# Kernel optimization log

Measured on AMD Instinct MI355X. Metric: run time of the kernel, lower is better.

Reference implementation:

```python
import jax, jax.numpy as jnp
import numpy as np

N_NODES = 100000
N_EDGES = 1600000
VOCAB = 10000
HIDDEN = 128
EMB1 = 128
EMB2 = 128
L1 = 64
N_GRAPHS = 256


def setup_inputs() -> dict:
    key = jax.random.key(0)
    ks = jax.random.split(key, 16)
    inp = {
        "x": jax.random.randint(ks[0], (N_NODES,), 0, VOCAB, dtype=jnp.int32),
        "edge_index": jax.random.randint(ks[1], (2, N_EDGES), 0, N_NODES, dtype=jnp.int32),
        "edge_weight": jax.random.uniform(ks[2], (N_EDGES,), dtype=jnp.float32),
        "batch": jnp.sort(jax.random.randint(ks[3], (N_NODES,), 0, N_GRAPHS, dtype=jnp.int32)),
        # parameters
        "emb_w": jax.random.normal(ks[4], (VOCAB, HIDDEN), dtype=jnp.float32) * 0.5,
        "w1_rel": jax.random.normal(ks[5], (EMB1, HIDDEN), dtype=jnp.float32) * (HIDDEN ** -0.5),
        "b1_rel": jnp.zeros((EMB1,), dtype=jnp.float32),
        "w1_root": jax.random.normal(ks[6], (EMB1, HIDDEN), dtype=jnp.float32) * (HIDDEN ** -0.5),
        "w2_rel": jax.random.normal(ks[7], (EMB2, EMB1), dtype=jnp.float32) * (EMB1 ** -0.5),
        "b2_rel": jnp.zeros((EMB2,), dtype=jnp.float32),
        "w2_root": jax.random.normal(ks[8], (EMB2, EMB1), dtype=jnp.float32) * (EMB1 ** -0.5),
        "cls1_w": jax.random.normal(ks[9], (L1, EMB2), dtype=jnp.float32) * (EMB2 ** -0.5),
        "cls1_b": jnp.zeros((L1,), dtype=jnp.float32),
        "cls2_w": jax.random.normal(ks[10], (2, L1), dtype=jnp.float32) * (L1 ** -0.5),
        "cls2_b": jnp.zeros((2,), dtype=jnp.float32),
    }
    return inp


def _embedding_max_norm(emb_w, idx, max_norm=1.0):
    # torch Embedding(max_norm=1): looked-up rows are renormalized to norm <= 1
    rows = emb_w[idx]                                        # [N, H]
    norm = jnp.linalg.norm(rows, axis=-1, keepdims=True)
    scale = jnp.minimum(1.0, max_norm / (norm + 1e-7))
    return rows * scale


def _graph_conv(h, src, dst, ew, w_rel, b_rel, w_root):
    # PyG GraphConv: out = lin_rel(sum_{j->i} w_ji * x_j) + lin_root(x_i)
    msg = h[src] * ew[:, None]                               # [E, D] gather
    agg = jax.ops.segment_sum(msg, dst, num_segments=N_NODES)  # [N, D] scatter-add
    return agg @ w_rel.T + b_rel + h @ w_root.T


def reference(x, edge_index, edge_weight, batch, emb_w,
              w1_rel, b1_rel, w1_root, w2_rel, b2_rel, w2_root,
              cls1_w, cls1_b, cls2_w, cls2_b):
    src, dst = edge_index[0], edge_index[1]
    h = _embedding_max_norm(emb_w, x)                        # [N, HIDDEN]
    # dropout is identity in eval mode
    h = jax.nn.relu(_graph_conv(h, src, dst, edge_weight, w1_rel, b1_rel, w1_root))
    h = jax.nn.relu(_graph_conv(h, src, dst, edge_weight, w2_rel, b2_rel, w2_root))
    # global mean pool over graphs
    sums = jax.ops.segment_sum(h, batch, num_segments=N_GRAPHS)        # [G, EMB2]
    counts = jax.ops.segment_sum(jnp.ones((h.shape[0],), h.dtype), batch,
                                 num_segments=N_GRAPHS)
    pooled = sums / jnp.maximum(counts, 1.0)[:, None]
    z = jax.nn.relu(pooled @ cls1_w.T + cls1_b)
    z = z @ cls2_w.T + cls2_b
    return jax.nn.softmax(z, axis=1)                          # [G, 2]
```

## Files before the change

kernel.cpp:

```cpp
#include <hip/hip_runtime.h>
#include <stdint.h>

#define NN 100000
#define NE 1600000
#define NG 256
#define NB 391
#define CHUNK 4096
#define NCH 391
#define NGS 392

typedef __attribute__((ext_vector_type(8))) short bf16x8;
typedef __attribute__((ext_vector_type(4))) float f32x4;

__device__ inline uint32_t f2bf(float f){
    uint32_t u = __float_as_uint(f);
    return (u + 0x7FFFu + ((u >> 16) & 1u)) >> 16;
}
__device__ inline float bflo(uint32_t u){ return __uint_as_float(u << 16); }
__device__ inline float bfhi(uint32_t u){ return __uint_as_float(u & 0xFFFF0000u); }
__device__ inline float bf1(short s){ return __uint_as_float(((uint32_t)(uint16_t)s) << 16); }

__global__ __launch_bounds__(256) void k_embed(const int* __restrict__ x,
                                               const float* __restrict__ emb,
                                               uint32_t* __restrict__ hout,
                                               const int* __restrict__ edst,
                                               int* __restrict__ bcnt,
                                               const int* __restrict__ batch,
                                               int* __restrict__ gstart,
                                               const float* __restrict__ w1rel, const float* __restrict__ w1root,
                                               const float* __restrict__ w2rel, const float* __restrict__ w2root,
                                               short* __restrict__ wf){
    int bid = blockIdx.x;
    if (bid < NN / 4){
        int w = threadIdx.x >> 6, l = threadIdx.x & 63;
        int n = bid * 4 + w;
        int r = x[n];
        const float2* e2 = (const float2*)emb;
        float2 v = e2[(size_t)r * 64 + l];
        float ss = v.x * v.x + v.y * v.y;
        #pragma unroll
        for (int off = 32; off; off >>= 1) ss += __shfl_xor(ss, off, 64);
        float sc = fminf(1.f, 1.f / (sqrtf(ss) + 1e-7f));
        hout[(size_t)n * 64 + l] = f2bf(v.x * sc) | (f2bf(v.y * sc) << 16);
    } else if (bid < NN / 4 + NCH){
        __shared__ int lh[NB];
        int t = threadIdx.x;
        int c0 = (bid - NN / 4) * CHUNK;
        int cnt = min(CHUNK, NE - c0);
        lh[t] = 0;
        if (t + 256 < NB) lh[t + 256] = 0;
        __syncthreads();
        for (int i = t; i < cnt; i += 256) atomicAdd(&lh[edst[c0 + i] >> 8], 1);
        __syncthreads();
        if (lh[t]) atomicAdd(&bcnt[t], lh[t]);
        if (t + 256 < NB && lh[t + 256]) atomicAdd(&bcnt[t + 256], lh[t + 256]);
    } else if (bid < NN / 4 + NCH + NGS){
        int i = (bid - NN / 4 - NCH) * 256 + threadIdx.x;
        if (i > NN) return;
        int bprev = (i == 0) ? -1 : batch[i - 1];
        int bcur  = (i == NN) ? NG : batch[i];
        for (int g = bprev + 1; g <= bcur; ++g) gstart[g] = i;
    } else {
        int id = (bid - NN / 4 - NCH - NGS) * 256 + threadIdx.x;
        int i = id & 7, lane = (id >> 3) & 63, ks = (id >> 9) & 3, j0 = (id >> 11) & 7, m = id >> 14;
        const float* W = (m == 0) ? w1rel : (m == 1) ? w1root : (m == 2) ? w2rel : w2root;
        int j = j0 * 16 + (lane & 15);
        int k = ks * 32 + (lane >> 4) * 8 + i;
        wf[id] = (short)f2bf(W[j * 128 + k]);
    }
}

__global__ __launch_bounds__(256) void k_bscatter(const int* __restrict__ esrc, const int* __restrict__ edst,
                                                  const float* __restrict__ ew,
                                                  const int* __restrict__ bcnt,
                                                  int* __restrict__ bbase, int* __restrict__ bfill,
                                                  uint2* __restrict__ cse2, int* __restrict__ ptrA){
    __shared__ uint2 rec[CHUNK];
    __shared__ unsigned short slotb[CHUNK];
    __shared__ int bb[512], hist[512], start[512], gbase[512], sc[512];
    int t = threadIdx.x;
    int g0 = (t < NB) ? bcnt[t] : 0;
    int g1 = (t + 256 < NB) ? bcnt[t + 256] : 0;
    sc[t] = g0; sc[t + 256] = g1;
    __syncthreads();
    for (int off = 1; off < 512; off <<= 1){
        int u0 = (t >= off) ? sc[t - off] : 0;
        int u1 = sc[t + 256 - off];
        __syncthreads();
        sc[t] += u0; sc[t + 256] += u1;
        __syncthreads();
    }
    bb[t] = sc[t] - g0; bb[t + 256] = sc[t + 256] - g1;
    if (t < NB) bbase[t] = bb[t];
    if (t + 256 < NB) bbase[t + 256] = bb[t + 256];
    if (t == 0){ bbase[NB] = NE; ptrA[NN] = NE; }
    hist[t] = 0; hist[t + 256] = 0;
    __syncthreads();
    int c0 = blockIdx.x * CHUNK;
    int cnt = min(CHUNK, NE - c0);
    for (int i = t; i < cnt; i += 256) atomicAdd(&hist[edst[c0 + i] >> 8], 1);
    __syncthreads();
    int v0 = hist[t], v1 = hist[t + 256];
    sc[t] = v0; sc[t + 256] = v1;
    __syncthreads();
    for (int off = 1; off < 512; off <<= 1){
        int u0 = (t >= off) ? sc[t - off] : 0;
        int u1 = sc[t + 256 - off];
        __syncthreads();
        sc[t] += u0; sc[t + 256] += u1;
        __syncthreads();
    }
    start[t] = sc[t] - v0;
    start[t + 256] = sc[t + 256] - v1;
    if (t < NB && v0 > 0) gbase[t] = bb[t] + atomicAdd(&bfill[t], v0);
    if (t + 256 < NB && v1 > 0) gbase[t + 256] = bb[t + 256] + atomicAdd(&bfill[t + 256], v1);
    __syncthreads();
    hist[t] = 0; hist[t + 256] = 0;
    __syncthreads();
    for (int i = t; i < cnt; i += 256){
        int d = edst[c0 + i];
        int b = d >> 8;
        int slot = start[b] + atomicAdd(&hist[b], 1);
        rec[slot] = make_uint2((uint32_t)esrc[c0 + i] | ((uint32_t)(d & 255) << 20),
                               __float_as_uint(ew[c0 + i]));
        slotb[slot] = (unsigned short)b;
    }
    __syncthreads();
    for (int i = t; i < cnt; i += 256){
        int b = slotb[i];
        cse2[gbase[b] + (i - start[b])] = rec[i];
    }
}

__global__ __launch_bounds__(256) void k_bcsr(const uint2* __restrict__ cse2,
                                              const int* __restrict__ bbase,
                                              int* __restrict__ ptrA,
                                              uint2* __restrict__ cse){
    __shared__ int cnt[256], sc[256], st[256];
    int t = threadIdx.x;
    int b = blockIdx.x;
    int ebase = bbase[b], eend = bbase[b + 1];
    int nb = b << 8;
    cnt[t] = 0;
    __syncthreads();
    for (int i = ebase + t; i < eend; i += 256){
        atomicAdd(&cnt[cse2[i].x >> 20], 1);
    }
    __syncthreads();
    int v = cnt[t];
    sc[t] = v;
    __syncthreads();
    for (int off = 1; off < 256; off <<= 1){
        int u = (t >= off) ? sc[t - off] : 0;
        __syncthreads();
        sc[t] += u;
        __syncthreads();
    }
    st[t] = sc[t] - v;
    if (nb + t < NN) ptrA[nb + t] = ebase + st[t];
    cnt[t] = 0;
    __syncthreads();
    for (int i = ebase + t; i < eend; i += 256){
        uint2 r = cse2[i];
        int dr = r.x >> 20;
        int pos = st[dr] + atomicAdd(&cnt[dr], 1);
        cse[ebase + pos] = make_uint2((r.x & 0xFFFFFu) << 8, r.y);
    }
}

#define ACC8(vv, ww) \
    a0 += ww * bflo(vv.x); a1 += ww * bfhi(vv.x); \
    a2 += ww * bflo(vv.y); a3 += ww * bfhi(vv.y); \
    a4 += ww * bflo(vv.z); a5 += ww * bfhi(vv.z); \
    a6 += ww * bflo(vv.w); a7 += ww * bfhi(vv.w);

__global__ __launch_bounds__(256) void k_agg(const uint32_t* __restrict__ hin,
                                             uint32_t* __restrict__ aggo,
                                             const int* __restrict__ ptr,
                                             const uint2* __restrict__ cse){
    int w = threadIdx.x >> 6, l = threadIdx.x & 63;
    int q = l >> 4, c = l & 15;
    int n = blockIdx.x * 4 + w;
    int p0 = ptr[n], p1 = ptr[n + 1];
    const char* hb = (const char*)hin;
    uint32_t coff = (uint32_t)(c << 4);
    float a0 = 0, a1 = 0, a2 = 0, a3 = 0, a4 = 0, a5 = 0, a6 = 0, a7 = 0;
    for (int base = p0; base < p1; base += 64){
        int m = p1 - base; if (m > 64) m = 64;
        int li = (l < m) ? l : (m - 1);
        uint2 rec = cse[base + li];
        int   myo = (int)rec.x;
        float myw = (l < m) ? __uint_as_float(rec.y) : 0.f;
        int e = 0;
        for (; e + 16 <= m; e += 16){
            int   o0 = __shfl(myo, e + q, 64);      float w0 = __shfl(myw, e + q, 64);
            int   o1 = __shfl(myo, e + 4 + q, 64);  float w1 = __shfl(myw, e + 4 + q, 64);
            int   o2 = __shfl(myo, e + 8 + q, 64);  float w2 = __shfl(myw, e + 8 + q, 64);
            int   o3 = __shfl(myo, e + 12 + q, 64); float w3 = __shfl(myw, e + 12 + q, 64);
            uint4 v0 = *(const uint4*)(hb + ((uint32_t)o0 + coff));
            uint4 v1 = *(const uint4*)(hb + ((uint32_t)o1 + coff));
            uint4 v2 = *(const uint4*)(hb + ((uint32_t)o2 + coff));
            uint4 v3 = *(const uint4*)(hb + ((uint32_t)o3 + coff));
            ACC8(v0, w0); ACC8(v1, w1); ACC8(v2, w2); ACC8(v3, w3);
        }
        for (; e < m; e += 4){
            int   o0 = __shfl(myo, e + q, 64);
            float w0 = __shfl(myw, e + q, 64);
            uint4 v0 = *(const uint4*)(hb + ((uint32_t)o0 + coff));
            ACC8(v0, w0);
        }
    }
    a0 += __shfl_xor(a0, 16, 64); a0 += __shfl_xor(a0, 32, 64);
    a1 += __shfl_xor(a1, 16, 64); a1 += __shfl_xor(a1, 32, 64);
    a2 += __shfl_xor(a2, 16, 64); a2 += __shfl_xor(a2, 32, 64);
    a3 += __shfl_xor(a3, 16, 64); a3 += __shfl_xor(a3, 32, 64);
    a4 += __shfl_xor(a4, 16, 64); a4 += __shfl_xor(a4, 32, 64);
    a5 += __shfl_xor(a5, 16, 64); a5 += __shfl_xor(a5, 32, 64);
    a6 += __shfl_xor(a6, 16, 64); a6 += __shfl_xor(a6, 32, 64);
    a7 += __shfl_xor(a7, 16, 64); a7 += __shfl_xor(a7, 32, 64);
    if (q == 0){
        uint4 o;
        o.x = f2bf(a0) | (f2bf(a1) << 16);
        o.y = f2bf(a2) | (f2bf(a3) << 16);
        o.z = f2bf(a4) | (f2bf(a5) << 16);
        o.w = f2bf(a6) | (f2bf(a7) << 16);
        *(uint4*)((char*)aggo + (size_t)n * 256 + coff) = o;
    }
}

__global__ __launch_bounds__(256) void k_gemm(const short* __restrict__ hin,
                                              const short* __restrict__ agg,
                                              short* __restrict__ hout,
                                              const bf16x8* __restrict__ wrel,
                                              const bf16x8* __restrict__ wroot,
                                              const float* __restrict__ bias){
    int t = threadIdx.x, w = t >> 6, l = t & 63;
    int rbase = blockIdx.x * 128 + w * 32;
    int r0 = rbase + (l & 15);
    int rA0 = min(r0, NN - 1);
    int rA1 = min(r0 + 16, NN - 1);
    int kb = (l >> 4) * 8;

    bf16x8 aA[2][4], aH[2][4];
    const short* pa0 = agg + (size_t)rA0 * 128 + kb;
    const short* pa1 = agg + (size_t)rA1 * 128 + kb;
    const short* ph0 = hin + (size_t)rA0 * 128 + kb;
    const short* ph1 = hin + (size_t)rA1 * 128 + kb;
    #pragma unroll
    for (int ks = 0; ks < 4; ++ks){
        aA[0][ks] = *(const bf16x8*)(pa0 + ks * 32);
        aA[1][ks] = *(const bf16x8*)(pa1 + ks * 32);
        aH[0][ks] = *(const bf16x8*)(ph0 + ks * 32);
        aH[1][ks] = *(const bf16x8*)(ph1 + ks * 32);
    }

    for (int j0 = 0; j0 < 8; ++j0){
        f32x4 acc0 = {0.f, 0.f, 0.f, 0.f}, acc1 = {0.f, 0.f, 0.f, 0.f};
        #pragma unroll
        for (int ks = 0; ks < 4; ++ks){
            bf16x8 br = wrel [(j0 * 4 + ks) * 64 + l];
            bf16x8 bo = wroot[(j0 * 4 + ks) * 64 + l];
            acc0 = __builtin_amdgcn_mfma_f32_16x16x32_bf16(aA[0][ks], br, acc0, 0, 0, 0);
            acc0 = __builtin_amdgcn_mfma_f32_16x16x32_bf16(aH[0][ks], bo, acc0, 0, 0, 0);
            acc1 = __builtin_amdgcn_mfma_f32_16x16x32_bf16(aA[1][ks], br, acc1, 0, 0, 0);
            acc1 = __builtin_amdgcn_mfma_f32_16x16x32_bf16(aH[1][ks], bo, acc1, 0, 0, 0);
        }
        int col = j0 * 16 + (l & 15);
        float bv = bias[col];
        int rb = rbase + (l >> 4) * 4;
        #pragma unroll
        for (int r = 0; r < 4; ++r){
            int row = rb + r;
            if (row < NN){
                float v = fmaxf(acc0[r] + bv, 0.f);
                hout[(size_t)row * 128 + col] = (short)f2bf(v);
            }
            int row1 = rb + 16 + r;
            if (row1 < NN){
                float v = fmaxf(acc1[r] + bv, 0.f);
                hout[(size_t)row1 * 128 + col] = (short)f2bf(v);
            }
        }
    }
}

__global__ __launch_bounds__(128) void k_poolcls(const short* __restrict__ h,
                                                 const int* __restrict__ gstart,
                                                 const float* __restrict__ c1w, const float* __restrict__ c1b,
                                                 const float* __restrict__ c2w, const float* __restrict__ c2b,
                                                 float* __restrict__ out){
    __shared__ float pl[128];
    __shared__ float z[64];
    __shared__ float logits[2];
    int g = blockIdx.x, t = threadIdx.x;
    int s = gstart[g], e = gstart[g + 1];
    float a0 = 0, a1 = 0, a2 = 0, a3 = 0;
    int i = s;
    for (; i + 3 < e; i += 4){
        a0 += bf1(h[(size_t)i * 128 + t]);
        a1 += bf1(h[(size_t)(i + 1) * 128 + t]);
        a2 += bf1(h[(size_t)(i + 2) * 128 + t]);
        a3 += bf1(h[(size_t)(i + 3) * 128 + t]);
    }
    for (; i < e; ++i) a0 += bf1(h[(size_t)i * 128 + t]);
    float sum = (a0 + a1) + (a2 + a3);
    int cnt = e - s;
    pl[t] = sum / fmaxf((float)cnt, 1.f);
    __syncthreads();
    if (t < 64){
        float acc = c1b[t];
        #pragma unroll 4
        for (int k = 0; k < 128; ++k) acc += pl[k] * c1w[t * 128 + k];
        z[t] = fmaxf(acc, 0.f);
    }
    __syncthreads();
    if (t < 2){
        float a = c2b[t];
        for (int k = 0; k < 64; ++k) a += z[k] * c2w[t * 64 + k];
        logits[t] = a;
    }
    __syncthreads();
    if (t == 0){
        float m = fmaxf(logits[0], logits[1]);
        float e0 = expf(logits[0] - m), e1 = expf(logits[1] - m);
        float ss = e0 + e1;
        out[g * 2 + 0] = e0 / ss;
        out[g * 2 + 1] = e1 / ss;
    }
}

extern "C" void kernel_launch(void* const* d_in, const int* in_sizes, int n_in,
                              void* d_out, int out_size, void* d_ws, size_t ws_size,
                              hipStream_t stream) {
    const int*   x      = (const int*)  d_in[0];
    const int*   eidx   = (const int*)  d_in[1];
    const float* ew     = (const float*)d_in[2];
    const int*   batch  = (const int*)  d_in[3];
    const float* emb    = (const float*)d_in[4];
    const float* w1rel  = (const float*)d_in[5];
    const float* b1     = (const float*)d_in[6];
    const float* w1root = (const float*)d_in[7];
    const float* w2rel  = (const float*)d_in[8];
    const float* b2     = (const float*)d_in[9];
    const float* w2root = (const float*)d_in[10];
    const float* c1w    = (const float*)d_in[11];
    const float* c1b    = (const float*)d_in[12];
    const float* c2w    = (const float*)d_in[13];
    const float* c2b    = (const float*)d_in[14];
    float* out = (float*)d_out;

    const int N = NN;
    const int E = NE;

    char* p = (char*)d_ws;
    auto alloc = [&](size_t bytes) -> void* {
        void* r = (void*)p;
        p += (bytes + 255) & ~(size_t)255;
        return r;
    };
    uint32_t* hA   = (uint32_t*)alloc((size_t)N * 64 * 4);
    uint32_t* hB   = (uint32_t*)alloc((size_t)N * 64 * 4);
    uint32_t* agg  = (uint32_t*)alloc((size_t)N * 64 * 4);
    int*   ptrA   = (int*)  alloc((size_t)(N + 1) * 4);
    int*   bcnt   = (int*)  alloc(NB * 4);
    int*   bbase  = (int*)  alloc((NB + 1) * 4);
    int*   bfill  = (int*)  alloc(NB * 4);
    uint2* cse2   = (uint2*)alloc((size_t)E * 8);
    uint2* cse    = (uint2*)alloc((size_t)E * 8);
    int*   gstart = (int*)  alloc((NG + 1) * 4);
    short* wf     = (short*)alloc(4 * 16384 * 2);
    (void)alloc(65536);

    const bf16x8* wf1rel  = (const bf16x8*)(wf);
    const bf16x8* wf1root = (const bf16x8*)(wf + 16384);
    const bf16x8* wf2rel  = (const bf16x8*)(wf + 32768);
    const bf16x8* wf2root = (const bf16x8*)(wf + 49152);

    const int* esrc = eidx;
    const int* edst = eidx + E;

    hipMemsetAsync(bcnt,  0, NB * 4, stream);
    hipMemsetAsync(bfill, 0, NB * 4, stream);

    k_embed<<<N / 4 + NCH + NGS + 256, 256, 0, stream>>>(x, emb, hA, edst, bcnt, batch, gstart,
                                                         w1rel, w1root, w2rel, w2root, wf);

    k_bscatter<<<NCH, 256, 0, stream>>>(esrc, edst, ew, bcnt, bbase, bfill, cse2, ptrA);
    k_bcsr    <<<NB,  256, 0, stream>>>(cse2, bbase, ptrA, cse);

    int ngemm = (N + 127) / 128;
    k_agg <<<N / 4, 256, 0, stream>>>(hA, agg, ptrA, cse);
    k_gemm<<<ngemm, 256, 0, stream>>>((const short*)hA, (const short*)agg, (short*)hB,
                                      wf1rel, wf1root, b1);
    k_agg <<<N / 4, 256, 0, stream>>>(hB, agg, ptrA, cse);
    k_gemm<<<ngemm, 256, 0, stream>>>((const short*)hB, (const short*)agg, (short*)hA,
                                      wf2rel, wf2root, b2);

    k_poolcls<<<NG, 128, 0, stream>>>((const short*)hA, gstart, c1w, c1b, c2w, c2b, out);
}
```

Measured before the change: 362.0 us.

## Fuse neighbor aggregation with GEMM through swizzled LDS tiles per block

Merges the gather-aggregate kernel and the MFMA GEMM kernel into one kernel. Each 256-thread block aggregates 16 nodes into LDS (bf16, XOR-swizzled), stages the nodes' own features there too, then runs the rel/root MFMAs with bias and ReLU. This removes the agg buffer's global write and re-read plus two launches per layer. It also prefetches the first CSR edge chunk for all four nodes of a wave up front. In exchange each block must reload the weight fragments from global/L2 (16 rows per block instead of 128), and a block barrier ties the GEMM to its slowest node's aggregation.

```diff
diff --git a/kernel.cpp b/kernel.cpp
--- a/kernel.cpp
+++ b/kernel.cpp
@@ -8,6 +8,7 @@
 #define CHUNK 4096
 #define NCH 391
 #define NGS 392
+#define NT 16
 
 typedef __attribute__((ext_vector_type(8))) short bf16x8;
 typedef __attribute__((ext_vector_type(4))) float f32x4;
@@ -174,112 +175,123 @@
     a4 += ww * bflo(vv.z); a5 += ww * bfhi(vv.z); \
     a6 += ww * bflo(vv.w); a7 += ww * bfhi(vv.w);
 
-__global__ __launch_bounds__(256) void k_agg(const uint32_t* __restrict__ hin,
-                                             uint32_t* __restrict__ aggo,
-                                             const int* __restrict__ ptr,
-                                             const uint2* __restrict__ cse){
-    int w = threadIdx.x >> 6, l = threadIdx.x & 63;
+__global__ __launch_bounds__(256) void k_aggemm(const uint32_t* __restrict__ hin,
+                                                short* __restrict__ hout,
+                                                const int* __restrict__ ptr,
+                                                const uint2* __restrict__ cse,
+                                                const bf16x8* __restrict__ wrel,
+                                                const bf16x8* __restrict__ wroot,
+                                                const float* __restrict__ bias){
+    __shared__ char ldsA[NT * 256];
+    __shared__ char ldsH[NT * 256];
+    int t = threadIdx.x, w = t >> 6, l = t & 63;
     int q = l >> 4, c = l & 15;
-    int n = blockIdx.x * 4 + w;
-    int p0 = ptr[n], p1 = ptr[n + 1];
+    int nb = blockIdx.x * NT;
+    int nw = nb + w * 4;
     const char* hb = (const char*)hin;
     uint32_t coff = (uint32_t)(c << 4);
-    float a0 = 0, a1 = 0, a2 = 0, a3 = 0, a4 = 0, a5 = 0, a6 = 0, a7 = 0;
-    for (int base = p0; base < p1; base += 64){
-        int m = p1 - base; if (m > 64) m = 64;
-        int li = (l < m) ? l : (m - 1);
-        uint2 rec = cse[base + li];
-        int   myo = (int)rec.x;
-        float myw = (l < m) ? __uint_as_float(rec.y) : 0.f;
-        int e = 0;
-        for (; e + 16 <= m; e += 16){
-            int   o0 = __shfl(myo, e + q, 64);      float w0 = __shfl(myw, e + q, 64);
-            int   o1 = __shfl(myo, e + 4 + q, 64);  float w1 = __shfl(myw, e + 4 + q, 64);
-            int   o2 = __shfl(myo, e + 8 + q, 64);  float w2 = __shfl(myw, e + 8 + q, 64);
-            int   o3 = __shfl(myo, e + 12 + q, 64); float w3 = __shfl(myw, e + 12 + q, 64);
-            uint4 v0 = *(const uint4*)(hb + ((uint32_t)o0 + coff));
-            uint4 v1 = *(const uint4*)(hb + ((uint32_t)o1 + coff));
-            uint4 v2 = *(const uint4*)(hb + ((uint32_t)o2 + coff));
-            uint4 v3 = *(const uint4*)(hb + ((uint32_t)o3 + coff));
-            ACC8(v0, w0); ACC8(v1, w1); ACC8(v2, w2); ACC8(v3, w3);
+
+    int p[5];
+    #pragma unroll
+    for (int tt = 0; tt < 5; ++tt) p[tt] = ptr[nw + tt];
+    uint2 rc[4];
+    int mm[4];
+    #pragma unroll
+    for (int tt = 0; tt < 4; ++tt){
+        int m = p[tt + 1] - p[tt]; if (m > 64) m = 64;
+        mm[tt] = m;
+        int li = (l < m) ? l : ((m > 0) ? m - 1 : 0);
+        int idx = p[tt] + li; if (idx > NE - 1) idx = NE - 1;
+        rc[tt] = cse[idx];
+    }
+    uint32_t ownv[4];
+    #pragma unroll
+    for (int tt = 0; tt < 4; ++tt) ownv[tt] = hin[(size_t)(nw + tt) * 64 + l];
+
+    #pragma unroll
+    for (int tt = 0; tt < 4; ++tt){
+        int row = w * 4 + tt;
+        float a0 = 0, a1 = 0, a2 = 0, a3 = 0, a4 = 0, a5 = 0, a6 = 0, a7 = 0;
+        auto run_chunk = [&](int myo, float myw, int m){
+            int e = 0;
+            for (; e + 16 <= m; e += 16){
+                int   o0 = __shfl(myo, e + q, 64);      float w0 = __shfl(myw, e + q, 64);
+                int   o1 = __shfl(myo, e + 4 + q, 64);  float w1 = __shfl(myw, e + 4 + q, 64);
+                int   o2 = __shfl(myo, e + 8 + q, 64);  float w2 = __shfl(myw, e + 8 + q, 64);
+                int   o3 = __shfl(myo, e + 12 + q, 64); float w3 = __shfl(myw, e + 12 + q, 64);
+                uint4 v0 = *(const uint4*)(hb + ((uint32_t)o0 + coff));
+                uint4 v1 = *(const uint4*)(hb + ((uint32_t)o1 + coff));
+                uint4 v2 = *(const uint4*)(hb + ((uint32_t)o2 + coff));
+                uint4 v3 = *(const uint4*)(hb + ((uint32_t)o3 + coff));
+                ACC8(v0, w0); ACC8(v1, w1); ACC8(v2, w2); ACC8(v3, w3);
+            }
+            for (; e < m; e += 4){
+                int   o0 = __shfl(myo, e + q, 64);
+                float w0 = __shfl(myw, e + q, 64);
+                uint4 v0 = *(const uint4*)(hb + ((uint32_t)o0 + coff));
+                ACC8(v0, w0);
+            }
+        };
+        {
+            int m = mm[tt];
+            int myo = (int)rc[tt].x;
+            float myw = (l < m) ? __uint_as_float(rc[tt].y) : 0.f;
+            run_chunk(myo, myw, m);
         }
-        for (; e < m; e += 4){
-            int   o0 = __shfl(myo, e + q, 64);
-            float w0 = __shfl(myw, e + q, 64);
-            uint4 v0 = *(const uint4*)(hb + ((uint32_t)o0 + coff));
-            ACC8(v0, w0);
+        for (int base = p[tt] + 64; base < p[tt + 1]; base += 64){
+            int m2 = p[tt + 1] - base; if (m2 > 64) m2 = 64;
+            int li2 = (l < m2) ? l : (m2 - 1);
+            uint2 r2 = cse[base + li2];
+            int myo = (int)r2.x;
+            float myw = (l < m2) ? __uint_as_float(r2.y) : 0.f;
+            run_chunk(myo, myw, m2);
         }
-    }
-    a0 += __shfl_xor(a0, 16, 64); a0 += __shfl_xor(a0, 32, 64);
-    a1 += __shfl_xor(a1, 16, 64); a1 += __shfl_xor(a1, 32, 64);
-    a2 += __shfl_xor(a2, 16, 64); a2 += __shfl_xor(a2, 32, 64);
-    a3 += __shfl_xor(a3, 16, 64); a3 += __shfl_xor(a3, 32, 64);
-    a4 += __shfl_xor(a4, 16, 64); a4 += __shfl_xor(a4, 32, 64);
-    a5 += __shfl_xor(a5, 16, 64); a5 += __shfl_xor(a5, 32, 64);
-    a6 += __shfl_xor(a6, 16, 64); a6 += __shfl_xor(a6, 32, 64);
-    a7 += __shfl_xor(a7, 16, 64); a7 += __shfl_xor(a7, 32, 64);
-    if (q == 0){
-        uint4 o;
-        o.x = f2bf(a0) | (f2bf(a1) << 16);
-        o.y = f2bf(a2) | (f2bf(a3) << 16);
-        o.z = f2bf(a4) | (f2bf(a5) << 16);
-        o.w = f2bf(a6) | (f2bf(a7) << 16);
-        *(uint4*)((char*)aggo + (size_t)n * 256 + coff) = o;
-    }
-}
-
-__global__ __launch_bounds__(256) void k_gemm(const short* __restrict__ hin,
-                                              const short* __restrict__ agg,
-                                              short* __restrict__ hout,
-                                              const bf16x8* __restrict__ wrel,
-                                              const bf16x8* __restrict__ wroot,
-                                              const float* __restrict__ bias){
-    int t = threadIdx.x, w = t >> 6, l = t & 63;
-    int rbase = blockIdx.x * 128 + w * 32;
-    int r0 = rbase + (l & 15);
-    int rA0 = min(r0, NN - 1);
-    int rA1 = min(r0 + 16, NN - 1);
-    int kb = (l >> 4) * 8;
-
-    bf16x8 aA[2][4], aH[2][4];
-    const short* pa0 = agg + (size_t)rA0 * 128 + kb;
-    const short* pa1 = agg + (size_t)rA1 * 128 + kb;
-    const short* ph0 = hin + (size_t)rA0 * 128 + kb;
-    const short* ph1 = hin + (size_t)rA1 * 128 + kb;
+        a0 += __shfl_xor(a0, 16, 64); a0 += __shfl_xor(a0, 32, 64);
+        a1 += __shfl_xor(a1, 16, 64); a1 += __shfl_xor(a1, 32, 64);
+        a2 += __shfl_xor(a2, 16, 64); a2 += __shfl_xor(a2, 32, 64);
+        a3 += __shfl_xor(a3, 16, 64); a3 += __shfl_xor(a3, 32, 64);
+        a4 += __shfl_xor(a4, 16, 64); a4 += __shfl_xor(a4, 32, 64);
+        a5 += __shfl_xor(a5, 16, 64); a5 += __shfl_xor(a5, 32, 64);
+        a6 += __shfl_xor(a6, 16, 64); a6 += __shfl_xor(a6, 32, 64);
+        a7 += __shfl_xor(a7, 16, 64); a7 += __shfl_xor(a7, 32, 64);
+        uint32_t swz = (uint32_t)((row & 7) << 4);
+        if (q == 0){
+            uint4 o;
+            o.x = f2bf(a0) | (f2bf(a1) << 16);
+            o.y = f2bf(a2) | (f2bf(a3) << 16);
+            o.z = f2bf(a4) | (f2bf(a5) << 16);
+            o.w = f2bf(a6) | (f2bf(a7) << 16);
+            *(uint4*)(ldsA + row * 256 + (int)(coff ^ swz)) = o;
+        }
+        *(uint32_t*)(ldsH + row * 256 + (int)(((uint32_t)(l * 4)) ^ swz)) = ownv[tt];
+    }
+    __syncthreads();
+
+    int r = l & 15, kq = l >> 4;
+    uint32_t rswz = (uint32_t)((r & 7) << 4);
+    bf16x8 aA[4], aH[4];
     #pragma unroll
     for (int ks = 0; ks < 4; ++ks){
-        aA[0][ks] = *(const bf16x8*)(pa0 + ks * 32);
-        aA[1][ks] = *(const bf16x8*)(pa1 + ks * 32);
-        aH[0][ks] = *(const bf16x8*)(ph0 + ks * 32);
-        aH[1][ks] = *(const bf16x8*)(ph1 + ks * 32);
-    }
-
-    for (int j0 = 0; j0 < 8; ++j0){
-        f32x4 acc0 = {0.f, 0.f, 0.f, 0.f}, acc1 = {0.f, 0.f, 0.f, 0.f};
+        uint32_t byte = (uint32_t)(ks * 64 + kq * 16);
+        aA[ks] = *(const bf16x8*)(ldsA + r * 256 + (int)(byte ^ rswz));
+        aH[ks] = *(const bf16x8*)(ldsH + r * 256 + (int)(byte ^ rswz));
+    }
+    #pragma unroll
+    for (int jj = 0; jj < 2; ++jj){
+        int j0 = w * 2 + jj;
+        f32x4 acc = {0.f, 0.f, 0.f, 0.f};
         #pragma unroll
         for (int ks = 0; ks < 4; ++ks){
-            bf16x8 br = wrel [(j0 * 4 + ks) * 64 + l];
-            bf16x8 bo = wroot[(j0 * 4 + ks) * 64 + l];
-            acc0 = __builtin_amdgcn_mfma_f32_16x16x32_bf16(aA[0][ks], br, acc0, 0, 0, 0);
-            acc0 = __builtin_amdgcn_mfma_f32_16x16x32_bf16(aH[0][ks], bo, acc0, 0, 0, 0);
-            acc1 = __builtin_amdgcn_mfma_f32_16x16x32_bf16(aA[1][ks], br, acc1, 0, 0, 0);
-            acc1 = __builtin_amdgcn_mfma_f32_16x16x32_bf16(aH[1][ks], bo, acc1, 0, 0, 0);
+            acc = __builtin_amdgcn_mfma_f32_16x16x32_bf16(aA[ks], wrel [(j0 * 4 + ks) * 64 + l], acc, 0, 0, 0);
+            acc = __builtin_amdgcn_mfma_f32_16x16x32_bf16(aH[ks], wroot[(j0 * 4 + ks) * 64 + l], acc, 0, 0, 0);
         }
-        int col = j0 * 16 + (l & 15);
+        int col = j0 * 16 + r;
         float bv = bias[col];
-        int rb = rbase + (l >> 4) * 4;
+        int rb = kq * 4;
         #pragma unroll
-        for (int r = 0; r < 4; ++r){
-            int row = rb + r;
-            if (row < NN){
-                float v = fmaxf(acc0[r] + bv, 0.f);
-                hout[(size_t)row * 128 + col] = (short)f2bf(v);
-            }
-            int row1 = rb + 16 + r;
-            if (row1 < NN){
-                float v = fmaxf(acc1[r] + bv, 0.f);
-                hout[(size_t)row1 * 128 + col] = (short)f2bf(v);
-            }
+        for (int rr = 0; rr < 4; ++rr){
+            float v = fmaxf(acc[rr] + bv, 0.f);
+            hout[(size_t)(nb + rb + rr) * 128 + col] = (short)f2bf(v);
         }
     }
 }
@@ -360,7 +372,6 @@
     };
     uint32_t* hA   = (uint32_t*)alloc((size_t)N * 64 * 4);
     uint32_t* hB   = (uint32_t*)alloc((size_t)N * 64 * 4);
-    uint32_t* agg  = (uint32_t*)alloc((size_t)N * 64 * 4);
     int*   ptrA   = (int*)  alloc((size_t)(N + 1) * 4);
     int*   bcnt   = (int*)  alloc(NB * 4);
     int*   bbase  = (int*)  alloc((NB + 1) * 4);
@@ -388,13 +399,8 @@
     k_bscatter<<<NCH, 256, 0, stream>>>(esrc, edst, ew, bcnt, bbase, bfill, cse2, ptrA);
     k_bcsr    <<<NB,  256, 0, stream>>>(cse2, bbase, ptrA, cse);
 
-    int ngemm = (N + 127) / 128;
-    k_agg <<<N / 4, 256, 0, stream>>>(hA, agg, ptrA, cse);
-    k_gemm<<<ngemm, 256, 0, stream>>>((const short*)hA, (const short*)agg, (short*)hB,
-                                      wf1rel, wf1root, b1);
-    k_agg <<<N / 4, 256, 0, stream>>>(hB, agg, ptrA, cse);
-    k_gemm<<<ngemm, 256, 0, stream>>>((const short*)hB, (const short*)agg, (short*)hA,
-                                      wf2rel, wf2root, b2);
+    k_aggemm<<<N / NT, 256, 0, stream>>>(hA, (short*)hB, ptrA, cse, wf1rel, wf1root, b1);
+    k_aggemm<<<N / NT, 256, 0, stream>>>(hB, (short*)hA, ptrA, cse, wf2rel, wf2root, b2);
 
     k_poolcls<<<NG, 128, 0, stream>>>((const short*)hA, gstart, c1w, c1b, c2w, c2b, out);
 }
```

New measurement: 379.7 us. 1.05x slower.
